# Kernel optimization log

Measured on AMD Instinct MI355X. Metric: run time of the kernel, lower is better.

The kernel has to match this reference:

```python
import jax, jax.numpy as jnp
import numpy as np

D = 512        # latent_dim
DT = 256       # text_latent_dim
H = 8          # num_heads
TE = 2048      # time_embed_dim
NEG = -1000000.0


def _ln(x, g, b, eps=1e-5):
    m = jnp.mean(x, axis=-1, keepdims=True)
    v = jnp.mean(jnp.square(x - m), axis=-1, keepdims=True)
    return (x - m) * jax.lax.rsqrt(v + eps) * g + b


def _linear(x, W, b):
    return x @ W.T + b


def setup_inputs() -> dict:
    key = jax.random.key(0)
    ks = jax.random.split(key, 24)
    B, T, NT, R, LR = 32, 1024, 77, 4, 256
    inp = {
        'x': jax.random.normal(ks[0], (B, T, D), jnp.float32),
        'xf': jax.random.normal(ks[1], (B, NT, DT), jnp.float32),
        'emb': jax.random.normal(ks[2], (B, TE), jnp.float32),
        'src_mask': jax.random.randint(ks[3], (B, T, 1), 0, 2).astype(jnp.float32),
        'cond_type': jax.random.randint(ks[4], (B, 1, 1), 0, 100).astype(jnp.int32),
        're_motion': jax.random.normal(ks[5], (B, R, LR, D), jnp.float32),
        're_text': jax.random.normal(ks[6], (B, R, 1, D), jnp.float32),
        're_mask': jax.random.randint(ks[7], (B, R, LR), 0, 2).astype(jnp.float32),
    }
    s = 0.02
    def W(k, o, i):
        return jax.random.normal(k, (o, i), jnp.float32) * s
    params = {
        'norm_g': jnp.ones((D,), jnp.float32), 'norm_b': jnp.zeros((D,), jnp.float32),
        'tnorm_g': jnp.ones((DT,), jnp.float32), 'tnorm_b': jnp.zeros((DT,), jnp.float32),
        'rn1_g': jnp.ones((2 * D,), jnp.float32), 'rn1_b': jnp.zeros((2 * D,), jnp.float32),
        'rn2_g': jnp.ones((D,), jnp.float32), 'rn2_b': jnp.zeros((D,), jnp.float32),
        'Wq': W(ks[8], D, D), 'bq': jnp.zeros((D,), jnp.float32),
        'Wkt': W(ks[9], D, DT), 'bkt': jnp.zeros((D,), jnp.float32),
        'Wvt': W(ks[10], D, DT), 'bvt': jnp.zeros((D,), jnp.float32),
        'Wkm': W(ks[11], D, D), 'bkm': jnp.zeros((D,), jnp.float32),
        'Wvm': W(ks[12], D, D), 'bvm': jnp.zeros((D,), jnp.float32),
        'Wkr': W(ks[13], D, 2 * D), 'bkr': jnp.zeros((D,), jnp.float32),
        'Wvr': W(ks[14], D, D), 'bvr': jnp.zeros((D,), jnp.float32),
        'emb_W': W(ks[15], 2 * D, TE), 'emb_b': jnp.zeros((2 * D,), jnp.float32),
        'snorm_g': jnp.ones((D,), jnp.float32), 'snorm_b': jnp.zeros((D,), jnp.float32),
        'out_W': W(ks[16], D, D), 'out_b': jnp.zeros((D,), jnp.float32),
    }
    inp.update(params)
    return inp


def _forward(x, xf, emb, src_mask, cond_type, re_motion, re_text, re_mask,
             norm_g, norm_b, tnorm_g, tnorm_b, rn1_g, rn1_b, rn2_g, rn2_b,
             Wq, bq, Wkt, bkt, Wvt, bvt, Wkm, bkm, Wvm, bvm, Wkr, bkr, Wvr, bvr,
             emb_W, emb_b, snorm_g, snorm_b, out_W, out_b):
    B, T, _ = x.shape
    re_mask_r = re_mask.reshape(B, -1, 1)                       # [B, R*LR, 1]
    N = xf.shape[1] + T + re_motion.shape[1] * re_motion.shape[2]

    xn = _ln(x, norm_g, norm_b)                                  # [B,T,D]
    xfn = _ln(xf, tnorm_g, tnorm_b)                              # [B,NT,DT]
    query = _linear(xn, Wq, bq)                                  # [B,T,D]

    text_ct = (cond_type % 10 > 0).astype(x.dtype)               # [B,1,1]
    retr_ct = (cond_type // 10 > 0).astype(x.dtype)              # [B,1,1]

    re_text_rep = jnp.broadcast_to(re_text, re_motion.shape)     # repeat along Lr
    re_feat_key = jnp.concatenate([re_motion, re_text_rep], axis=-1).reshape(B, -1, 2 * D)

    k_text = _linear(xfn, Wkt, bkt) + (1.0 - text_ct) * NEG
    k_retr = (_linear(_ln(re_feat_key, rn1_g, rn1_b), Wkr, bkr)
              + (1.0 - retr_ct) * NEG + (1.0 - re_mask_r) * NEG)
    k_mot = _linear(xn, Wkm, bkm) + (1.0 - src_mask) * NEG
    key_cat = jnp.concatenate([k_text, k_retr, k_mot], axis=1)   # [B,N,D]

    q = jax.nn.softmax(query.reshape(B, T, H, -1), axis=-1)      # softmax over head_dim
    k = jax.nn.softmax(key_cat.reshape(B, N, H, -1), axis=1)     # softmax over tokens

    re_feat_value = re_motion.reshape(B, -1, D)
    v_text = _linear(xfn, Wvt, bvt) * text_ct
    v_retr = _linear(_ln(re_feat_value, rn2_g, rn2_b), Wvr, bvr) * retr_ct * re_mask_r
    v_mot = _linear(xn, Wvm, bvm) * src_mask
    v = jnp.concatenate([v_text, v_retr, v_mot], axis=1).reshape(B, N, H, -1)

    attention = jnp.einsum('bnhd,bnhl->bhdl', k, v)              # [B,H,hd,hd]
    y = jnp.einsum('bthd,bhdl->bthl', q, attention).reshape(B, T, D)

    # StylizationBlock: film-style scale/shift from time embedding, zero-init out proj
    emb_out = _linear(jax.nn.silu(emb), emb_W, emb_b)[:, None, :]  # [B,1,2D]
    scale, shift = emb_out[..., :D], emb_out[..., D:]
    h = _ln(y, snorm_g, snorm_b) * (1.0 + scale) + shift
    h = _linear(jax.nn.silu(h), out_W, out_b)
    return x + h


def reference(x, xf, emb, src_mask, cond_type, re_motion, re_text, re_mask,
              norm_g, norm_b, tnorm_g, tnorm_b, rn1_g, rn1_b, rn2_g, rn2_b,
              Wq, bq, Wkt, bkt, Wvt, bvt, Wkm, bkm, Wvm, bvm, Wkr, bkr, Wvr, bvr,
              emb_W, emb_b, snorm_g, snorm_b, out_W, out_b):
    return _forward(x, xf, emb, src_mask, cond_type, re_motion, re_text, re_mask,
                    norm_g, norm_b, tnorm_g, tnorm_b, rn1_g, rn1_b, rn2_g, rn2_b,
                    Wq, bq, Wkt, bkt, Wvt, bvt, Wkm, bkm, Wvm, bvm, Wkr, bkr, Wvr, bvr,
                    emb_W, emb_b, snorm_g, snorm_b, out_W, out_b)
```

## Files before the change

### kernel.cpp

```cpp
#include <hip/hip_runtime.h>
#include <cstddef>
#include <cstdint>

#define DEV __device__ __forceinline__

namespace {

constexpr int kH = 8;
constexpr int kB = 32, kT = 1024, kNT = 77, kR = 4, kLR = 256;
constexpr int kRL = kR * kLR;
constexpr float kNEG = -1000000.0f;
constexpr int kNtot = 2304;
constexpr int kNS2 = 3;

typedef __bf16 bf16x8 __attribute__((ext_vector_type(8)));
typedef float f32x4 __attribute__((ext_vector_type(4)));

DEV unsigned short f2bf(float f) {
  unsigned int u = __float_as_uint(f);
  u += 0x7fffu + ((u >> 16) & 1u);
  return (unsigned short)(u >> 16);
}
DEV float bf2f(unsigned short h) { return __uint_as_float(((unsigned int)h) << 16); }

DEV float wave_sum(float v) {
  #pragma unroll
  for (int s = 32; s; s >>= 1) v += __shfl_xor(v, s);
  return v;
}

template<int COLS>
__global__ __launch_bounds__(256) void ln_bf16(const float* __restrict__ in,
    const float* __restrict__ g, const float* __restrict__ be,
    unsigned short* __restrict__ out) {
  constexpr int PT = COLS / 256;
  int row = blockIdx.x;
  const float* p = in + (size_t)row * COLS;
  unsigned short* o = out + (size_t)row * COLS;
  float v[PT]; float s = 0.f, s2 = 0.f;
  #pragma unroll
  for (int i = 0; i < PT; i++) {
    v[i] = p[threadIdx.x + i * 256];
    s += v[i]; s2 += v[i] * v[i];
  }
  __shared__ float red[2][4];
  int lane = threadIdx.x & 63, w = threadIdx.x >> 6;
  s = wave_sum(s); s2 = wave_sum(s2);
  if (!lane) { red[0][w] = s; red[1][w] = s2; }
  __syncthreads();
  s = red[0][0] + red[0][1] + red[0][2] + red[0][3];
  s2 = red[1][0] + red[1][1] + red[1][2] + red[1][3];
  float mean = s / COLS;
  float var = s2 / COLS - mean * mean;
  float rstd = rsqrtf(var + 1e-5f);
  #pragma unroll
  for (int i = 0; i < PT; i++) {
    int c = threadIdx.x + i * 256;
    o[c] = f2bf((v[i] - mean) * rstd * g[c] + be[c]);
  }
}

__global__ __launch_bounds__(256) void rfk_stats(const float* __restrict__ mot,
    const float* __restrict__ txt, unsigned short* __restrict__ mot_bf,
    float* __restrict__ s1k, float* __restrict__ s2k,
    float* __restrict__ s1v, float* __restrict__ s2v) {
  int m = blockIdx.x;
  const float* pm = mot + (size_t)m * 512;
  const float* pt = txt + (size_t)(m >> 8) * 512;
  float v[2], t[2];
  float sv = 0.f, sv2 = 0.f, st = 0.f, st2 = 0.f;
  #pragma unroll
  for (int i = 0; i < 2; i++) {
    v[i] = pm[threadIdx.x + i * 256]; sv += v[i]; sv2 += v[i] * v[i];
    t[i] = pt[threadIdx.x + i * 256]; st += t[i]; st2 += t[i] * t[i];
  }
  __shared__ float red[4][4];
  int lane = threadIdx.x & 63, w = threadIdx.x >> 6;
  sv = wave_sum(sv); sv2 = wave_sum(sv2); st = wave_sum(st); st2 = wave_sum(st2);
  if (!lane) { red[0][w] = sv; red[1][w] = sv2; red[2][w] = st; red[3][w] = st2; }
  __syncthreads();
  #pragma unroll
  for (int i = 0; i < 2; i++)
    mot_bf[(size_t)m * 512 + threadIdx.x + i * 256] = f2bf(v[i]);
  if (threadIdx.x == 0) {
    float SV = red[0][0] + red[0][1] + red[0][2] + red[0][3];
    float SV2 = red[1][0] + red[1][1] + red[1][2] + red[1][3];
    float ST = red[2][0] + red[2][1] + red[2][2] + red[2][3];
    float ST2 = red[3][0] + red[3][1] + red[3][2] + red[3][3];
    float SA = SV + ST, SA2 = SV2 + ST2;
    float ma = SA / 1024.f, va = SA2 / 1024.f - ma * ma;
    float ra = rsqrtf(va + 1e-5f);
    float mv = SV / 512.f, vv = SV2 / 512.f - mv * mv;
    float rv = rsqrtf(vv + 1e-5f);
    s1k[m] = ra; s2k[m] = -ra * ma;
    s1v[m] = rv; s2v[m] = -rv * mv;
  }
}

__global__ __launch_bounds__(256) void prep_w(
    const float* __restrict__ Wkr, const float* __restrict__ g1,
    const float* __restrict__ b1, const float* __restrict__ bkr,
    const float* __restrict__ Wvr, const float* __restrict__ g2,
    const float* __restrict__ b2, const float* __restrict__ bvr,
    unsigned short* __restrict__ w1lo, unsigned short* __restrict__ w2,
    float* __restrict__ G1, float* __restrict__ B1,
    float* __restrict__ G2, float* __restrict__ B2) {
  int n = blockIdx.x;
  int tid = threadIdx.x;
  float gs = 0.f, bs = 0.f;
  #pragma unroll
  for (int i = 0; i < 4; i++) {
    int k = tid + i * 256;
    float w = Wkr[(size_t)n * 1024 + k];
    float gv = g1[k];
    gs += gv * w; bs += b1[k] * w;
    if (i < 2) w1lo[(size_t)n * 512 + k] = f2bf(gv * w);
  }
  float g2s = 0.f, b2s = 0.f;
  #pragma unroll
  for (int i = 0; i < 2; i++) {
    int k = tid + i * 256;
    float w = Wvr[(size_t)n * 512 + k];
    g2s += g2[k] * w; b2s += b2[k] * w;
    w2[(size_t)n * 512 + k] = f2bf(g2[k] * w);
  }
  __shared__ float red[4][4];
  int lane = tid & 63, w_ = tid >> 6;
  gs = wave_sum(gs); bs = wave_sum(bs); g2s = wave_sum(g2s); b2s = wave_sum(b2s);
  if (!lane) { red[0][w_] = gs; red[1][w_] = bs; red[2][w_] = g2s; red[3][w_] = b2s; }
  __syncthreads();
  if (tid == 0) {
    G1[n] = red[0][0] + red[0][1] + red[0][2] + red[0][3];
    B1[n] = red[1][0] + red[1][1] + red[1][2] + red[1][3] + bkr[n];
    G2[n] = red[2][0] + red[2][1] + red[2][2] + red[2][3];
    B2[n] = red[3][0] + red[3][1] + red[3][2] + red[3][3] + bvr[n];
  }
}

__global__ __launch_bounds__(256) void text_T(const float* __restrict__ re_text,
    const float* __restrict__ g1, const float* __restrict__ Wkr,
    float* __restrict__ T) {
  int m = blockIdx.x;
  int ns = blockIdx.y;
  __shared__ float tr[512];
  int tid = threadIdx.x;
  #pragma unroll
  for (int i = 0; i < 2; i++) {
    int k = tid + i * 256;
    tr[k] = re_text[(size_t)m * 512 + k] * g1[512 + k];
  }
  __syncthreads();
  int n = ns * 64 + (tid >> 2);
  int k0 = (tid & 3) * 128;
  const float* wp = Wkr + (size_t)n * 1024 + 512 + k0;
  float acc = 0.f;
  #pragma unroll
  for (int k = 0; k < 128; k += 4) {
    float4 w4 = *reinterpret_cast<const float4*>(wp + k);
    float4 t4 = *reinterpret_cast<const float4*>(&tr[k0 + k]);
    acc = fmaf(t4.x, w4.x, fmaf(t4.y, w4.y, fmaf(t4.z, w4.z, fmaf(t4.w, w4.w, acc))));
  }
  acc += __shfl_xor(acc, 1);
  acc += __shfl_xor(acc, 2);
  if ((tid & 3) == 0) T[(size_t)m * 512 + n] = acc;
}

__global__ __launch_bounds__(256) void rowmask_kernel(const int* __restrict__ ct,
    const float* __restrict__ src_mask, const float* __restrict__ re_mask,
    float* __restrict__ kaT, float* __restrict__ kaR, float* __restrict__ kaM,
    float* __restrict__ vmT, float* __restrict__ vmR, float* __restrict__ vmM,
    int nB) {
  int i = blockIdx.x * 256 + threadIdx.x;
  if (i < nB * kRL) {
    int b = i >> 10;
    int c = ct[b];
    float retr = (c / 10 > 0) ? 1.f : 0.f;
    float rm = re_mask[i];
    kaR[i] = (1.f - retr) * kNEG + (1.f - rm) * kNEG;
    vmR[i] = retr * rm;
    float sm = src_mask[i];
    kaM[i] = (1.f - sm) * kNEG;
    vmM[i] = sm;
  }
  if (i < nB * kNT) {
    int b = i / kNT;
    int c = ct[b];
    float text = (c % 10 > 0) ? 1.f : 0.f;
    kaT[i] = (1.f - text) * kNEG;
    vmT[i] = text;
  }
}

__global__ __launch_bounds__(256) void castw(const float* __restrict__ s,
    unsigned short* __restrict__ d, int n) {
  int i = (blockIdx.x * 256 + threadIdx.x) * 4;
  if (i < n) {
    float4 v = *reinterpret_cast<const float4*>(s + i);
    ushort4 o;
    o.x = f2bf(v.x); o.y = f2bf(v.y); o.z = f2bf(v.z); o.w = f2bf(v.w);
    *reinterpret_cast<ushort4*>(d + i) = o;
  }
}

__global__ __launch_bounds__(256) void zpad_kernel(unsigned short* __restrict__ E,
    unsigned short* __restrict__ V, int rows) {
  int i = blockIdx.x * 256 + threadIdx.x;
  if (i >= rows * 24) return;
  int row = i / 24, c = i % 24;
  size_t off = (size_t)row * kNtot + 2112 + c * 8;
  ulonglong2 z; z.x = 0; z.y = 0;
  *reinterpret_cast<ulonglong2*>(E + off) = z;
  *reinterpret_cast<ulonglong2*>(V + off) = z;
}

__global__ __launch_bounds__(256) void silu_emb(const float* __restrict__ emb,
    float* __restrict__ semb) {
  int i = (blockIdx.x * 256 + threadIdx.x) * 4;
  float4 v = *reinterpret_cast<const float4*>(emb + i);
  float4 o;
  o.x = v.x / (1.f + __expf(-v.x));
  o.y = v.y / (1.f + __expf(-v.y));
  o.z = v.z / (1.f + __expf(-v.z));
  o.w = v.w / (1.f + __expf(-v.w));
  *reinterpret_cast<float4*>(semb + i) = o;
}

__global__ __launch_bounds__(256) void emb_gemv2(const float* __restrict__ semb,
    const float* __restrict__ W, float* __restrict__ part) {
  int n = blockIdx.x * 4 + (threadIdx.x >> 6);
  int s = blockIdx.y;
  int lane = threadIdx.x & 63;
  int k = s * 256 + lane * 4;
  float4 wv = *reinterpret_cast<const float4*>(&W[(size_t)n * 2048 + k]);
  float acc[32];
  #pragma unroll
  for (int m = 0; m < 32; m++) {
    float4 sv = *reinterpret_cast<const float4*>(&semb[(size_t)m * 2048 + k]);
    acc[m] = fmaf(sv.x, wv.x, fmaf(sv.y, wv.y, fmaf(sv.z, wv.z, sv.w * wv.w)));
  }
  #pragma unroll
  for (int m = 0; m < 32; m++) {
    float t = wave_sum(acc[m]);
    if (lane == 0) part[((size_t)s * 32 + m) * 1024 + n] = t;
  }
}
__global__ __launch_bounds__(256) void emb_fin(const float* __restrict__ part,
    const float* __restrict__ bias, float* __restrict__ ss) {
  int i = blockIdx.x * 256 + threadIdx.x;
  float s = 0.f;
  #pragma unroll
  for (int c = 0; c < 8; c++) s += part[(size_t)c * 32768 + i];
  ss[i] = s + bias[i & 1023];
}

__global__ __launch_bounds__(256) void res_kernel(const unsigned short* __restrict__ c,
    const float* __restrict__ x, float* __restrict__ out, int n4) {
  for (int i = blockIdx.x * 256 + threadIdx.x; i < n4; i += gridDim.x * 256) {
    int j = i * 4;
    ushort4 cv = *reinterpret_cast<const ushort4*>(c + j);
    float4 xv = *reinterpret_cast<const float4*>(x + j);
    float4 o;
    o.x = xv.x + bf2f(cv.x); o.y = xv.y + bf2f(cv.y);
    o.z = xv.z + bf2f(cv.z); o.w = xv.w + bf2f(cv.w);
    *reinterpret_cast<float4*>(out + j) = o;
  }
}

template<int OUTMODE, int TR, int EPI>
__global__ __launch_bounds__(256) void gemm_mfma(
    const unsigned short* __restrict__ A, const unsigned short* __restrict__ W,
    const float* __restrict__ bias, void* __restrict__ Cout,
    int M, int K, int m_per_b, int n_total, int out_off,
    const float* __restrict__ rowAdd, const float* __restrict__ rowMul,
    const float* __restrict__ s1, const float* __restrict__ s2,
    const float* __restrict__ Gv, const float* __restrict__ Tt) {
  __shared__ __align__(16) char smem[32768];
  unsigned short* lds = (unsigned short*)smem;
  const int tid = threadIdx.x;
  const int lane = tid & 63;
  const int wv = tid >> 6;
  const int wr = (wv >> 1) * 64;
  const int wc = (wv & 1) * 64;
  const int m0 = blockIdx.y * 128;
  const int n0 = blockIdx.x * 128;

  const unsigned short* srcA[2]; const unsigned short* srcB[2];
  int dstOff[2];
  #pragma unroll
  for (int i = 0; i < 2; i++) {
    int lin = i * 256 + tid;
    int r = lin >> 2, cl = lin & 3;
    int cs = cl ^ ((r >> 1) & 3);
    int ra = m0 + r; if (ra > M - 1) ra = M - 1;
    srcA[i] = A + (size_t)ra * K + cs * 8;
    srcB[i] = W + (size_t)(n0 + r) * K + cs * 8;
    dstOff[i] = lin * 8;
  }
  int offA[4], offB[4];
  #pragma unroll
  for (int i = 0; i < 4; i++) {
    int r = wr + i * 16 + (lane & 15);
    int c = (lane >> 4) ^ ((r >> 1) & 3);
    offA[i] = r * 32 + c * 8;
    int rb = wc + i * 16 + (lane & 15);
    int cb = (lane >> 4) ^ ((rb >> 1) & 3);
    offB[i] = rb * 32 + cb * 8;
  }

  f32x4 acc[4][4] = {};

  #pragma unroll
  for (int i = 0; i < 2; i++) {
    __builtin_amdgcn_global_load_lds(
        (const __attribute__((address_space(1))) void*)(srcA[i]),
        (__attribute__((address_space(3))) void*)&lds[dstOff[i]], 16, 0, 0);
    __builtin_amdgcn_global_load_lds(
        (const __attribute__((address_space(1))) void*)(srcB[i]),
        (__attribute__((address_space(3))) void*)&lds[4096 + dstOff[i]], 16, 0, 0);
  }
  __syncthreads();

  int c = 0;
  for (int k0 = 0; k0 < K; k0 += 32) {
    int nc = c ^ 1;
    if (k0 + 32 < K) {
      #pragma unroll
      for (int i = 0; i < 2; i++) {
        __builtin_amdgcn_global_load_lds(
            (const __attribute__((address_space(1))) void*)(srcA[i] + k0 + 32),
            (__attribute__((address_space(3))) void*)&lds[nc * 8192 + dstOff[i]], 16, 0, 0);
        __builtin_amdgcn_global_load_lds(
            (const __attribute__((address_space(1))) void*)(srcB[i] + k0 + 32),
            (__attribute__((address_space(3))) void*)&lds[nc * 8192 + 4096 + dstOff[i]], 16, 0, 0);
      }
    }
    bf16x8 af[4], bf[4];
    #pragma unroll
    for (int i = 0; i < 4; i++) {
      af[i] = *reinterpret_cast<const bf16x8*>(&lds[c * 8192 + offA[i]]);
      bf[i] = *reinterpret_cast<const bf16x8*>(&lds[c * 8192 + 4096 + offB[i]]);
    }
    #pragma unroll
    for (int i = 0; i < 4; i++)
      #pragma unroll
      for (int j = 0; j < 4; j++)
        acc[i][j] = __builtin_amdgcn_mfma_f32_16x16x32_bf16(af[i], bf[j], acc[i][j], 0, 0, 0);
    __syncthreads();
    c = nc;
  }

  const int r4 = (lane >> 4) << 2;
  const int colb = n0 + wc + (lane & 15);
  const int rowb = m0 + wr + r4;

  auto epival = [&](float accv, int rowg, int col) -> float {
    float v;
    if (EPI == 1) {
      v = (accv + Tt[(size_t)(rowg >> 8) * 512 + col]) * s1[rowg]
          + s2[rowg] * Gv[col] + bias[col] + rowAdd[rowg];
    } else if (EPI == 2) {
      v = (accv * s1[rowg] + s2[rowg] * Gv[col] + bias[col]) * rowMul[rowg];
    } else {
      float ra = rowAdd ? rowAdd[rowg] : 0.f;
      float rm = rowMul ? rowMul[rowg] : 1.f;
      v = (accv + bias[col] + ra) * rm;
    }
    if (OUTMODE == 2) v = __expf(v);
    return v;
  };

  if (TR && (m_per_b & 7)) {
    unsigned short* C16 = (unsigned short*)Cout;
    #pragma unroll
    for (int i = 0; i < 4; i++) {
      #pragma unroll
      for (int r = 0; r < 4; r++) {
        int row = rowb + i * 16 + r;
        if (row >= M) continue;
        size_t nn = out_off + (row % m_per_b);
        size_t cb = (size_t)(row / m_per_b) * 512;
        #pragma unroll
        for (int j = 0; j < 4; j++) {
          int col = colb + j * 16;
          C16[(cb + col) * kNtot + nn] = f2bf(epival(acc[i][j][r], row, col));
        }
      }
    }
    return;
  }

  unsigned short* S = (unsigned short*)smem;
  #pragma unroll
  for (int i = 0; i < 4; i++) {
    #pragma unroll
    for (int r = 0; r < 4; r++) {
      int row_t = wr + i * 16 + r4 + r;
      int rowg = m0 + row_t; if (rowg > M - 1) rowg = M - 1;
      int key = ((row_t >> 3) & 7) << 3;
      #pragma unroll
      for (int j = 0; j < 4; j++) {
        int col_t = wc + j * 16 + (lane & 15);
        S[row_t * 128 + (col_t ^ key)] = f2bf(epival(acc[i][j][r], rowg, n0 + col_t));
      }
    }
  }
  __syncthreads();
  if (TR) {
    #pragma unroll
    for (int it = 0; it < 8; it++) {
      int slot = it * 256 + tid;
      int col_t = slot >> 4;
      int mcx = slot & 15;
      int mc = mcx * 8;
      int key = (mcx & 7) << 3;
      union { unsigned short u[8]; ulonglong2 v; } w;
      #pragma unroll
      for (int e = 0; e < 8; e++)
        w.u[e] = S[(mc + e) * 128 + (col_t ^ key)];
      int row = m0 + mc;
      size_t obase = ((size_t)(row / m_per_b) * 512 + n0 + col_t) * (size_t)kNtot
                   + out_off + (row % m_per_b);
      *reinterpret_cast<ulonglong2*>((unsigned short*)Cout + obase) = w.v;
    }
  } else {
    #pragma unroll
    for (int it = 0; it < 8; it++) {
      int slot = it * 256 + tid;
      int row_t = slot >> 4;
      int cs = (slot & 15) * 8;
      int key = ((row_t >> 3) & 7) << 3;
      int row = m0 + row_t;
      if (row < M) {
        size_t orow = (size_t)(row / m_per_b) * n_total + out_off + (row % m_per_b);
        ulonglong2 d = *reinterpret_cast<const ulonglong2*>(&S[row_t * 128 + (cs ^ key)]);
        *reinterpret_cast<ulonglong2*>((unsigned short*)Cout + orow * 512 + n0 + cs) = d;
      }
    }
  }
}

__global__ __launch_bounds__(256) void attp_kernel(const unsigned short* __restrict__ E,
    const unsigned short* __restrict__ V, float* __restrict__ part,
    float* __restrict__ part_cs) {
  int bh = blockIdx.x;
  int s = blockIdx.y;
  const unsigned short* Ep = E + (size_t)bh * 64 * kNtot;
  const unsigned short* Vp = V + (size_t)bh * 64 * kNtot;
  __shared__ __align__(16) char smem[34816];
  unsigned short* Elds = (unsigned short*)smem;
  unsigned short* Vlds = (unsigned short*)(smem + 17408);
  int tid = threadIdx.x, lane = tid & 63, wv = tid >> 6;
  f32x4 acc[4] = {};
  float csum = 0.f;
  int cd = tid & 63, cq = tid >> 6;
  const int arow = (wv * 16 + (lane & 15)) * 136 + ((lane >> 4) << 3);
  const int brow0 = ((lane & 15)) * 136 + ((lane >> 4) << 3);

  for (int it = 0; it < 6; it++) {
    int n0 = s * 768 + it * 128;
    __syncthreads();
    #pragma unroll
    for (int r = 0; r < 4; r++) {
      int ch = r * 256 + tid;
      int d = ch >> 4, off = (ch & 15) * 8;
      *reinterpret_cast<ulonglong2*>(&Elds[d * 136 + off]) =
          *reinterpret_cast<const ulonglong2*>(Ep + (size_t)d * kNtot + n0 + off);
      *reinterpret_cast<ulonglong2*>(&Vlds[d * 136 + off]) =
          *reinterpret_cast<const ulonglong2*>(Vp + (size_t)d * kNtot + n0 + off);
    }
    __syncthreads();
    #pragma unroll
    for (int ks = 0; ks < 4; ks++) {
      bf16x8 af = *reinterpret_cast<const bf16x8*>(&Elds[arow + ks * 32]);
      #pragma unroll
      for (int j = 0; j < 4; j++) {
        bf16x8 bf = *reinterpret_cast<const bf16x8*>(&Vlds[brow0 + j * 16 * 136 + ks * 32]);
        acc[j] = __builtin_amdgcn_mfma_f32_16x16x32_bf16(af, bf, acc[j], 0, 0, 0);
      }
    }
    #pragma unroll
    for (int k8 = 0; k8 < 4; k8++) {
      bf16x8 ev = *reinterpret_cast<const bf16x8*>(&Elds[cd * 136 + cq * 32 + k8 * 8]);
      const unsigned short* pu = reinterpret_cast<const unsigned short*>(&ev);
      #pragma unroll
      for (int e = 0; e < 8; e++) csum += bf2f(pu[e]);
    }
  }
  float* op = part + ((size_t)bh * kNS2 + s) * 4096;
  int dbase = wv * 16 + ((lane >> 4) << 2);
  #pragma unroll
  for (int j = 0; j < 4; j++)
    #pragma unroll
    for (int r = 0; r < 4; r++)
      op[(dbase + r) * 64 + j * 16 + (lane & 15)] = acc[j][r];
  __syncthreads();
  float* csu = (float*)smem;
  csu[cq * 64 + cd] = csum;
  __syncthreads();
  if (tid < 64)
    part_cs[((size_t)bh * kNS2 + s) * 64 + tid] =
        csu[tid] + csu[64 + tid] + csu[128 + tid] + csu[192 + tid];
}

__global__ __launch_bounds__(256) void attc_kernel(const float* __restrict__ part,
    const float* __restrict__ part_cs, unsigned short* __restrict__ attT) {
  int bh = blockIdx.x;
  __shared__ float at[64][65];
  __shared__ float sinv[64];
  int tid = threadIdx.x;
  if (tid < 64) {
    float s = 0.f;
    #pragma unroll
    for (int c = 0; c < kNS2; c++) s += part_cs[((size_t)bh * kNS2 + c) * 64 + tid];
    sinv[tid] = 1.f / s;
  }
  for (int i = tid; i < 4096; i += 256) {
    float s = 0.f;
    #pragma unroll
    for (int c = 0; c < kNS2; c++) s += part[((size_t)bh * kNS2 + c) * 4096 + i];
    at[i >> 6][i & 63] = s;
  }
  __syncthreads();
  for (int j = tid; j < 4096; j += 256) {
    int l = j >> 6, d = j & 63;
    attT[(size_t)bh * 4096 + j] = f2bf(at[d][l] * sinv[d]);
  }
}

__global__ __launch_bounds__(256) void y_mfma(const unsigned short* __restrict__ q,
    const unsigned short* __restrict__ attT, unsigned short* __restrict__ y) {
  int bh = blockIdx.x; int b = bh >> 3, h = bh & 7;
  int t0 = blockIdx.y * 128;
  __shared__ unsigned short bt[64][72];
  __shared__ float rs[128];
  __shared__ unsigned short ob[128][72];
  int tid = threadIdx.x, lane = tid & 63, wv = tid >> 6;
  int wr = wv * 32;
  for (int i = tid; i < 512; i += 256) {
    int row = i >> 3, c8 = (i & 7) * 8;
    *reinterpret_cast<ulonglong2*>(&bt[row][c8]) =
        *reinterpret_cast<const ulonglong2*>(attT + (size_t)bh * 4096 + row * 64 + c8);
  }
  const unsigned short* qp = q + ((size_t)(b * 1024 + t0 + wr)) * 512 + h * 64;
  bf16x8 af[2][2];
  #pragma unroll
  for (int i = 0; i < 2; i++) {
    int row = i * 16 + (lane & 15);
    #pragma unroll
    for (int s = 0; s < 2; s++)
      af[i][s] = *reinterpret_cast<const bf16x8*>(qp + (size_t)row * 512 + s * 32 + (lane >> 4) * 8);
  }
  #pragma unroll
  for (int i = 0; i < 2; i++) {
    float r = 0.f;
    #pragma unroll
    for (int s = 0; s < 2; s++) {
      const unsigned short* pu = reinterpret_cast<const unsigned short*>(&af[i][s]);
      #pragma unroll
      for (int e = 0; e < 8; e++) r += bf2f(pu[e]);
    }
    r += __shfl_xor(r, 16); r += __shfl_xor(r, 32);
    if (lane < 16) rs[wr + i * 16 + lane] = r;
  }
  __syncthreads();
  f32x4 acc[2][4] = {};
  #pragma unroll
  for (int s = 0; s < 2; s++) {
    #pragma unroll
    for (int j = 0; j < 4; j++) {
      bf16x8 bf = *reinterpret_cast<const bf16x8*>(&bt[j * 16 + (lane & 15)][s * 32 + (lane >> 4) * 8]);
      #pragma unroll
      for (int i = 0; i < 2; i++)
        acc[i][j] = __builtin_amdgcn_mfma_f32_16x16x32_bf16(af[i][s], bf, acc[i][j], 0, 0, 0);
    }
  }
  int r4 = (lane >> 4) << 2;
  #pragma unroll
  for (int i = 0; i < 2; i++) {
    #pragma unroll
    for (int r = 0; r < 4; r++) {
      int row = wr + i * 16 + r4 + r;
      float rinv = 1.f / rs[row];
      #pragma unroll
      for (int j = 0; j < 4; j++)
        ob[row][j * 16 + (lane & 15)] = f2bf(acc[i][j][r] * rinv);
    }
  }
  __syncthreads();
  for (int i = tid; i < 1024; i += 256) {
    int row = i >> 3, c8 = (i & 7) * 8;
    *reinterpret_cast<ulonglong2*>(y + ((size_t)(b * 1024 + t0 + row)) * 512 + h * 64 + c8) =
        *reinterpret_cast<const ulonglong2*>(&ob[row][c8]);
  }
}

__global__ __launch_bounds__(256) void mod_kernel(const unsigned short* __restrict__ y,
    const float* __restrict__ ss, const float* __restrict__ g, const float* __restrict__ be,
    unsigned short* __restrict__ h) {
  int row = blockIdx.x; int b = row >> 10;
  const unsigned short* p = y + (size_t)row * 512;
  unsigned short* o = h + (size_t)row * 512;
  float v[2]; float s = 0.f, s2 = 0.f;
  #pragma unroll
  for (int i = 0; i < 2; i++) {
    v[i] = bf2f(p[threadIdx.x + i * 256]);
    s += v[i]; s2 += v[i] * v[i];
  }
  __shared__ float red[2][4];
  int lane = threadIdx.x & 63, w = threadIdx.x >> 6;
  s = wave_sum(s); s2 = wave_sum(s2);
  if (!lane) { red[0][w] = s; red[1][w] = s2; }
  __syncthreads();
  s = red[0][0] + red[0][1] + red[0][2] + red[0][3];
  s2 = red[1][0] + red[1][1] + red[1][2] + red[1][3];
  float mean = s / 512.f, var = s2 / 512.f - mean * mean;
  float rstd = rsqrtf(var + 1e-5f);
  #pragma unroll
  for (int i = 0; i < 2; i++) {
    int c = threadIdx.x + i * 256;
    float val = (v[i] - mean) * rstd * g[c] + be[c];
    val = val * (1.f + ss[b * 1024 + c]) + ss[b * 1024 + 512 + c];
    o[c] = f2bf(val / (1.f + __expf(-val)));
  }
}

}

extern "C" void kernel_launch(void* const* d_in, const int* in_sizes, int n_in,
                              void* d_out, int out_size, void* d_ws, size_t ws_size,
                              hipStream_t stream) {
  const float* x        = (const float*)d_in[0];
  const float* xf       = (const float*)d_in[1];
  const float* emb      = (const float*)d_in[2];
  const float* src_mask = (const float*)d_in[3];
  const int*   cond     = (const int*)d_in[4];
  const float* re_motion= (const float*)d_in[5];
  const float* re_text  = (const float*)d_in[6];
  const float* re_mask  = (const float*)d_in[7];
  const float* norm_g = (const float*)d_in[8],  * norm_b = (const float*)d_in[9];
  const float* tnorm_g= (const float*)d_in[10], * tnorm_b= (const float*)d_in[11];
  const float* rn1_g  = (const float*)d_in[12], * rn1_b  = (const float*)d_in[13];
  const float* rn2_g  = (const float*)d_in[14], * rn2_b  = (const float*)d_in[15];
  const float* Wq  = (const float*)d_in[16], * bq  = (const float*)d_in[17];
  const float* Wkt = (const float*)d_in[18], * bkt = (const float*)d_in[19];
  const float* Wvt = (const float*)d_in[20], * bvt = (const float*)d_in[21];
  const float* Wkm = (const float*)d_in[22], * bkm = (const float*)d_in[23];
  const float* Wvm = (const float*)d_in[24], * bvm = (const float*)d_in[25];
  const float* Wkr = (const float*)d_in[26], * bkr = (const float*)d_in[27];
  const float* Wvr = (const float*)d_in[28], * bvr = (const float*)d_in[29];
  const float* emb_W = (const float*)d_in[30], * emb_b = (const float*)d_in[31];
  const float* snorm_g = (const float*)d_in[32], * snorm_b = (const float*)d_in[33];
  const float* out_W = (const float*)d_in[34], * out_b = (const float*)d_in[35];
  float* out = (float*)d_out;

  char* base = (char*)d_ws;
  size_t off = 0;
  auto ab = [&](size_t nb) { char* p = base + off; off = (off + nb + 255) & ~(size_t)255; return p; };

  unsigned short* wq_bf  = (unsigned short*)ab(512 * 512 * 2);
  unsigned short* wkt_bf = (unsigned short*)ab(512 * 256 * 2);
  unsigned short* wvt_bf = (unsigned short*)ab(512 * 256 * 2);
  unsigned short* wkm_bf = (unsigned short*)ab(512 * 512 * 2);
  unsigned short* wvm_bf = (unsigned short*)ab(512 * 512 * 2);
  unsigned short* wout_bf= (unsigned short*)ab(512 * 512 * 2);
  unsigned short* w1lo_bf= (unsigned short*)ab(512 * 512 * 2);
  unsigned short* w2_bf  = (unsigned short*)ab(512 * 512 * 2);
  float* G1 = (float*)ab(512 * 4); float* B1 = (float*)ab(512 * 4);
  float* G2 = (float*)ab(512 * 4); float* B2 = (float*)ab(512 * 4);
  float* Tbuf = (float*)ab((size_t)kB * kR * 512 * 4);
  float* semb_f   = (float*)ab((size_t)kB * 2048 * 4);
  float* part_emb = (float*)ab((size_t)8 * kB * 1024 * 4);
  float* ssb_full = (float*)ab((size_t)kB * 1024 * 4);
  float* kaT_full = (float*)ab((size_t)kB * kNT * 4);
  float* vmT_full = (float*)ab((size_t)kB * kNT * 4);
  float* kaR_full = (float*)ab((size_t)kB * kRL * 4);
  float* kaM_full = (float*)ab((size_t)kB * kT * 4);
  float* vmR_full = (float*)ab((size_t)kB * kRL * 4);
  float* vmM_full = (float*)ab((size_t)kB * kT * 4);
  const size_t fixed_off = off;

  auto pad = [](size_t n) { return (n + 255) & ~(size_t)255; };
  auto att_bytes = [&](size_t CH) -> size_t {
    return pad(CH * 8 * 4096 * 2)
         + pad(CH * 8 * (size_t)kNS2 * 4096 * 4)
         + pad(CH * 8 * (size_t)kNS2 * 64 * 4);
  };
  auto chunk_bytes = [&](size_t CH) -> size_t {
    size_t xnr = pad(CH * 1024 * 512 * 2);
    if (att_bytes(CH) > xnr) xnr = att_bytes(CH);
    size_t s = 0;
    s += xnr;
    s += pad(CH * kNT * 256 * 2);
    s += pad(CH * 1024 * 512 * 2);
    s += 4 * pad(CH * 1024 * 4);
    s += pad(CH * 1024 * 512 * 2);
    s += pad((size_t)CH * 512 * kNtot * 2);
    s += pad((size_t)CH * 512 * kNtot * 2);
    return s;
  };
  int CH = 32;
  while (CH > 1 && fixed_off + chunk_bytes(CH) > ws_size) CH >>= 1;

  auto cl = [&](const float* s, unsigned short* d, int n) {
    castw<<<dim3((n / 4 + 255) / 256), 256, 0, stream>>>(s, d, n);
  };
  cl(Wq,  wq_bf,  512 * 512);
  cl(Wkt, wkt_bf, 512 * 256);
  cl(Wvt, wvt_bf, 512 * 256);
  cl(Wkm, wkm_bf, 512 * 512);
  cl(Wvm, wvm_bf, 512 * 512);
  cl(out_W, wout_bf, 512 * 512);
  prep_w<<<dim3(512), 256, 0, stream>>>(Wkr, rn1_g, rn1_b, bkr, Wvr, rn2_g, rn2_b, bvr,
                                        w1lo_bf, w2_bf, G1, B1, G2, B2);
  text_T<<<dim3(kB * kR, 8), 256, 0, stream>>>(re_text, rn1_g, Wkr, Tbuf);

  rowmask_kernel<<<dim3(kB * 4), 256, 0, stream>>>(cond, src_mask, re_mask,
      kaT_full, kaR_full, kaM_full, vmT_full, vmR_full, vmM_full, kB);
  silu_emb<<<dim3(kB * 2048 / 1024), 256, 0, stream>>>(emb, semb_f);
  emb_gemv2<<<dim3(256, 8), 256, 0, stream>>>(semb_f, emb_W, part_emb);
  emb_fin<<<dim3(128), 256, 0, stream>>>(part_emb, emb_b, ssb_full);

  for (int b0 = 0; b0 < kB; b0 += CH) {
    off = fixed_off;
    const int MRc = CH * 1024;
    const int MTc = CH * kNT;

    size_t xnr = pad((size_t)MRc * 512 * 2);
    if (att_bytes(CH) > xnr) xnr = att_bytes(CH);
    char* xnR = ab(xnr);
    unsigned short* xn_bf  = (unsigned short*)xnR;
    unsigned short* attT = (unsigned short*)xnR;
    float* attp = (float*)(xnR + pad((size_t)CH * 8 * 4096 * 2));
    float* part_cs = (float*)(xnR + pad((size_t)CH * 8 * 4096 * 2)
                                  + pad((size_t)CH * 8 * (size_t)kNS2 * 4096 * 4));
    unsigned short* h_bf = xn_bf;

    unsigned short* xfn_bf = (unsigned short*)ab((size_t)MTc * 256 * 2);
    unsigned short* mot_bf = (unsigned short*)ab((size_t)MRc * 512 * 2);
    float* s1k = (float*)ab((size_t)CH * 1024 * 4);
    float* s2k = (float*)ab((size_t)CH * 1024 * 4);
    float* s1v = (float*)ab((size_t)CH * 1024 * 4);
    float* s2v = (float*)ab((size_t)CH * 1024 * 4);
    unsigned short* qb_bf  = (unsigned short*)ab((size_t)MRc * 512 * 2);
    unsigned short* kc_bf  = (unsigned short*)ab((size_t)CH * 512 * kNtot * 2);
    unsigned short* vb_bf  = (unsigned short*)ab((size_t)CH * 512 * kNtot * 2);
    unsigned short* yb16 = mot_bf;
    unsigned short* cfin = qb_bf;

    const float* x_c   = x + (size_t)b0 * kT * 512;
    const float* xf_c  = xf + (size_t)b0 * kNT * 256;
    const float* rm_c  = re_motion + (size_t)b0 * kRL * 512;
    const float* rt_c  = re_text + (size_t)b0 * kR * 512;
    float* out_c = out + (size_t)b0 * kT * 512;

    ln_bf16<512><<<dim3(MRc), 256, 0, stream>>>(x_c, norm_g, norm_b, xn_bf);
    ln_bf16<256><<<dim3(MTc), 256, 0, stream>>>(xf_c, tnorm_g, tnorm_b, xfn_bf);
    rfk_stats<<<dim3(MRc), 256, 0, stream>>>(rm_c, rt_c, mot_bf, s1k, s2k, s1v, s2v);
    zpad_kernel<<<dim3(CH * 48), 256, 0, stream>>>(kc_bf, vb_bf, CH * 512);

    gemm_mfma<2, 0, 0><<<dim3(4, CH * 8), 256, 0, stream>>>(xn_bf, wq_bf, bq, qb_bf,
        MRc, 512, MRc, 0, 0, nullptr, nullptr, nullptr, nullptr, nullptr, nullptr);
    gemm_mfma<2, 1, 0><<<dim3(4, (MTc + 127) / 128), 256, 0, stream>>>(xfn_bf, wkt_bf, bkt, kc_bf,
        MTc, 256, kNT, 0, 0, kaT_full + (size_t)b0 * kNT, nullptr,
        nullptr, nullptr, nullptr, nullptr);
    gemm_mfma<2, 1, 1><<<dim3(4, CH * 8), 256, 0, stream>>>(mot_bf, w1lo_bf, B1, kc_bf,
        MRc, 512, kRL, 0, kNT, kaR_full + (size_t)b0 * kRL, nullptr,
        s1k, s2k, G1, Tbuf + (size_t)b0 * kR * 512);
    gemm_mfma<2, 1, 0><<<dim3(4, CH * 8), 256, 0, stream>>>(xn_bf, wkm_bf, bkm, kc_bf,
        MRc, 512, kT, 0, kNT + kRL, kaM_full + (size_t)b0 * kT, nullptr,
        nullptr, nullptr, nullptr, nullptr);
    gemm_mfma<1, 1, 0><<<dim3(4, (MTc + 127) / 128), 256, 0, stream>>>(xfn_bf, wvt_bf, bvt, vb_bf,
        MTc, 256, kNT, 0, 0, nullptr, vmT_full + (size_t)b0 * kNT,
        nullptr, nullptr, nullptr, nullptr);
    gemm_mfma<1, 1, 2><<<dim3(4, CH * 8), 256, 0, stream>>>(mot_bf, w2_bf, B2, vb_bf,
        MRc, 512, kRL, 0, kNT, nullptr, vmR_full + (size_t)b0 * kRL,
        s1v, s2v, G2, nullptr);
    gemm_mfma<1, 1, 0><<<dim3(4, CH * 8), 256, 0, stream>>>(xn_bf, wvm_bf, bvm, vb_bf,
        MRc, 512, kT, 0, kNT + kRL, nullptr, vmM_full + (size_t)b0 * kT,
        nullptr, nullptr, nullptr, nullptr);

    attp_kernel<<<dim3(CH * 8, kNS2), 256, 0, stream>>>(kc_bf, vb_bf, attp, part_cs);
    attc_kernel<<<dim3(CH * 8), 256, 0, stream>>>(attp, part_cs, attT);
    y_mfma<<<dim3(CH * 8, 8), 256, 0, stream>>>(qb_bf, attT, yb16);

    mod_kernel<<<dim3(MRc), 256, 0, stream>>>(yb16, ssb_full + (size_t)b0 * 1024,
                                              snorm_g, snorm_b, h_bf);
    gemm_mfma<1, 0, 0><<<dim3(4, CH * 8), 256, 0, stream>>>(h_bf, wout_bf, out_b, cfin,
        MRc, 512, MRc, 0, 0, nullptr, nullptr, nullptr, nullptr, nullptr, nullptr);
    res_kernel<<<dim3(2048), 256, 0, stream>>>(cfin, x_c, out_c, MRc * 128);
  }
}
```

Baseline: 563.8 us.

## Fuse projection GEMMs sharing an input into concatenated-weight launches

Concatenates the weights of projections that share the same activation input (Q/Km/Vm on the normalized motion, K/V retrieval on the motion features, K/V text on the text features). Each group becomes one wider GEMM whose column section picks the per-section epilogue and output buffer. This cuts seven GEMM launches to three and gives each launch a larger grid, in exchange for a templated kernel with section-dependent branching. The output GEMM gets a separate, simplified kernel. The A tile is still reloaded for each N tile, so the reuse gain is mostly from fewer launches and fuller grids.

```diff
diff --git a/kernel.cpp b/kernel.cpp
--- a/kernel.cpp
+++ b/kernel.cpp
@@ -266,14 +266,19 @@
   }
 }
 
-template<int OUTMODE, int TR, int EPI>
-__global__ __launch_bounds__(256) void gemm_mfma(
+template<int COMBO>
+__global__ __launch_bounds__(256) void gemm_fused(
     const unsigned short* __restrict__ A, const unsigned short* __restrict__ W,
-    const float* __restrict__ bias, void* __restrict__ Cout,
-    int M, int K, int m_per_b, int n_total, int out_off,
-    const float* __restrict__ rowAdd, const float* __restrict__ rowMul,
-    const float* __restrict__ s1, const float* __restrict__ s2,
-    const float* __restrict__ Gv, const float* __restrict__ Tt) {
+    int M, int K, int m_per_b, int out_off,
+    unsigned short* __restrict__ qout,
+    unsigned short* __restrict__ E, unsigned short* __restrict__ V,
+    const float* __restrict__ biasA, const float* __restrict__ biasB,
+    const float* __restrict__ biasC,
+    const float* __restrict__ rowAddK, const float* __restrict__ rowMulV,
+    const float* __restrict__ s1k, const float* __restrict__ s2k,
+    const float* __restrict__ s1v, const float* __restrict__ s2v,
+    const float* __restrict__ G1v, const float* __restrict__ G2v,
+    const float* __restrict__ Tt) {
   __shared__ __align__(16) char smem[32768];
   unsigned short* lds = (unsigned short*)smem;
   const int tid = threadIdx.x;
@@ -283,6 +288,8 @@
   const int wc = (wv & 1) * 64;
   const int m0 = blockIdx.y * 128;
   const int n0 = blockIdx.x * 128;
+  const int sec = n0 >> 9;
+  const int nlo = n0 & 511;
 
   const unsigned short* srcA[2]; const unsigned short* srcB[2];
   int dstOff[2];
@@ -350,27 +357,27 @@
   }
 
   const int r4 = (lane >> 4) << 2;
-  const int colb = n0 + wc + (lane & 15);
   const int rowb = m0 + wr + r4;
 
-  auto epival = [&](float accv, int rowg, int col) -> float {
-    float v;
-    if (EPI == 1) {
-      v = (accv + Tt[(size_t)(rowg >> 8) * 512 + col]) * s1[rowg]
-          + s2[rowg] * Gv[col] + bias[col] + rowAdd[rowg];
-    } else if (EPI == 2) {
-      v = (accv * s1[rowg] + s2[rowg] * Gv[col] + bias[col]) * rowMul[rowg];
+  auto epival = [&](float accv, int rowg, int cl) -> float {
+    if (COMBO == 0) {
+      if (sec == 0) return __expf(accv + biasA[cl]);
+      if (sec == 1) return __expf(accv + biasB[cl] + rowAddK[rowg]);
+      return (accv + biasC[cl]) * rowMulV[rowg];
+    } else if (COMBO == 1) {
+      if (sec == 0)
+        return __expf((accv + Tt[(size_t)(rowg >> 8) * 512 + cl]) * s1k[rowg]
+                      + s2k[rowg] * G1v[cl] + biasA[cl] + rowAddK[rowg]);
+      return (accv * s1v[rowg] + s2v[rowg] * G2v[cl] + biasB[cl]) * rowMulV[rowg];
     } else {
-      float ra = rowAdd ? rowAdd[rowg] : 0.f;
-      float rm = rowMul ? rowMul[rowg] : 1.f;
-      v = (accv + bias[col] + ra) * rm;
-    }
-    if (OUTMODE == 2) v = __expf(v);
-    return v;
+      if (sec == 0) return __expf(accv + biasA[cl] + rowAddK[rowg]);
+      return (accv + biasB[cl]) * rowMulV[rowg];
+    }
   };
 
-  if (TR && (m_per_b & 7)) {
-    unsigned short* C16 = (unsigned short*)Cout;
+  unsigned short* dstEV = (COMBO == 0) ? (sec == 1 ? E : V) : (sec == 0 ? E : V);
+
+  if (COMBO == 2) {
     #pragma unroll
     for (int i = 0; i < 4; i++) {
       #pragma unroll
@@ -381,8 +388,8 @@
         size_t cb = (size_t)(row / m_per_b) * 512;
         #pragma unroll
         for (int j = 0; j < 4; j++) {
-          int col = colb + j * 16;
-          C16[(cb + col) * kNtot + nn] = f2bf(epival(acc[i][j][r], row, col));
+          int cl = nlo + wc + j * 16 + (lane & 15);
+          dstEV[(cb + cl) * kNtot + nn] = f2bf(epival(acc[i][j][r], row, cl));
         }
       }
     }
@@ -400,12 +407,26 @@
       #pragma unroll
       for (int j = 0; j < 4; j++) {
         int col_t = wc + j * 16 + (lane & 15);
-        S[row_t * 128 + (col_t ^ key)] = f2bf(epival(acc[i][j][r], rowg, n0 + col_t));
+        S[row_t * 128 + (col_t ^ key)] = f2bf(epival(acc[i][j][r], rowg, nlo + col_t));
       }
     }
   }
   __syncthreads();
-  if (TR) {
+  bool linear = (COMBO == 0 && sec == 0);
+  if (linear) {
+    #pragma unroll
+    for (int it = 0; it < 8; it++) {
+      int slot = it * 256 + tid;
+      int row_t = slot >> 4;
+      int cs = (slot & 15) * 8;
+      int key = ((row_t >> 3) & 7) << 3;
+      int row = m0 + row_t;
+      if (row < M) {
+        ulonglong2 d = *reinterpret_cast<const ulonglong2*>(&S[row_t * 128 + (cs ^ key)]);
+        *reinterpret_cast<ulonglong2*>(qout + (size_t)row * 512 + nlo + cs) = d;
+      }
+    }
+  } else {
     #pragma unroll
     for (int it = 0; it < 8; it++) {
       int slot = it * 256 + tid;
@@ -418,23 +439,118 @@
       for (int e = 0; e < 8; e++)
         w.u[e] = S[(mc + e) * 128 + (col_t ^ key)];
       int row = m0 + mc;
-      size_t obase = ((size_t)(row / m_per_b) * 512 + n0 + col_t) * (size_t)kNtot
+      size_t obase = ((size_t)(row / m_per_b) * 512 + nlo + col_t) * (size_t)kNtot
                    + out_off + (row % m_per_b);
-      *reinterpret_cast<ulonglong2*>((unsigned short*)Cout + obase) = w.v;
-    }
-  } else {
-    #pragma unroll
-    for (int it = 0; it < 8; it++) {
-      int slot = it * 256 + tid;
-      int row_t = slot >> 4;
-      int cs = (slot & 15) * 8;
+      *reinterpret_cast<ulonglong2*>(dstEV + obase) = w.v;
+    }
+  }
+}
+
+__global__ __launch_bounds__(256) void gemm_mfma(
+    const unsigned short* __restrict__ A, const unsigned short* __restrict__ W,
+    const float* __restrict__ bias, unsigned short* __restrict__ Cout,
+    int M, int K) {
+  __shared__ __align__(16) char smem[32768];
+  unsigned short* lds = (unsigned short*)smem;
+  const int tid = threadIdx.x;
+  const int lane = tid & 63;
+  const int wv = tid >> 6;
+  const int wr = (wv >> 1) * 64;
+  const int wc = (wv & 1) * 64;
+  const int m0 = blockIdx.y * 128;
+  const int n0 = blockIdx.x * 128;
+
+  const unsigned short* srcA[2]; const unsigned short* srcB[2];
+  int dstOff[2];
+  #pragma unroll
+  for (int i = 0; i < 2; i++) {
+    int lin = i * 256 + tid;
+    int r = lin >> 2, cl = lin & 3;
+    int cs = cl ^ ((r >> 1) & 3);
+    int ra = m0 + r; if (ra > M - 1) ra = M - 1;
+    srcA[i] = A + (size_t)ra * K + cs * 8;
+    srcB[i] = W + (size_t)(n0 + r) * K + cs * 8;
+    dstOff[i] = lin * 8;
+  }
+  int offA[4], offB[4];
+  #pragma unroll
+  for (int i = 0; i < 4; i++) {
+    int r = wr + i * 16 + (lane & 15);
+    int c = (lane >> 4) ^ ((r >> 1) & 3);
+    offA[i] = r * 32 + c * 8;
+    int rb = wc + i * 16 + (lane & 15);
+    int cb = (lane >> 4) ^ ((rb >> 1) & 3);
+    offB[i] = rb * 32 + cb * 8;
+  }
+
+  f32x4 acc[4][4] = {};
+
+  #pragma unroll
+  for (int i = 0; i < 2; i++) {
+    __builtin_amdgcn_global_load_lds(
+        (const __attribute__((address_space(1))) void*)(srcA[i]),
+        (__attribute__((address_space(3))) void*)&lds[dstOff[i]], 16, 0, 0);
+    __builtin_amdgcn_global_load_lds(
+        (const __attribute__((address_space(1))) void*)(srcB[i]),
+        (__attribute__((address_space(3))) void*)&lds[4096 + dstOff[i]], 16, 0, 0);
+  }
+  __syncthreads();
+
+  int c = 0;
+  for (int k0 = 0; k0 < K; k0 += 32) {
+    int nc = c ^ 1;
+    if (k0 + 32 < K) {
+      #pragma unroll
+      for (int i = 0; i < 2; i++) {
+        __builtin_amdgcn_global_load_lds(
+            (const __attribute__((address_space(1))) void*)(srcA[i] + k0 + 32),
+            (__attribute__((address_space(3))) void*)&lds[nc * 8192 + dstOff[i]], 16, 0, 0);
+        __builtin_amdgcn_global_load_lds(
+            (const __attribute__((address_space(1))) void*)(srcB[i] + k0 + 32),
+            (__attribute__((address_space(3))) void*)&lds[nc * 8192 + 4096 + dstOff[i]], 16, 0, 0);
+      }
+    }
+    bf16x8 af[4], bf[4];
+    #pragma unroll
+    for (int i = 0; i < 4; i++) {
+      af[i] = *reinterpret_cast<const bf16x8*>(&lds[c * 8192 + offA[i]]);
+      bf[i] = *reinterpret_cast<const bf16x8*>(&lds[c * 8192 + 4096 + offB[i]]);
+    }
+    #pragma unroll
+    for (int i = 0; i < 4; i++)
+      #pragma unroll
+      for (int j = 0; j < 4; j++)
+        acc[i][j] = __builtin_amdgcn_mfma_f32_16x16x32_bf16(af[i], bf[j], acc[i][j], 0, 0, 0);
+    __syncthreads();
+    c = nc;
+  }
+
+  const int r4 = (lane >> 4) << 2;
+  unsigned short* S = (unsigned short*)smem;
+  #pragma unroll
+  for (int i = 0; i < 4; i++) {
+    #pragma unroll
+    for (int r = 0; r < 4; r++) {
+      int row_t = wr + i * 16 + r4 + r;
       int key = ((row_t >> 3) & 7) << 3;
-      int row = m0 + row_t;
-      if (row < M) {
-        size_t orow = (size_t)(row / m_per_b) * n_total + out_off + (row % m_per_b);
-        ulonglong2 d = *reinterpret_cast<const ulonglong2*>(&S[row_t * 128 + (cs ^ key)]);
-        *reinterpret_cast<ulonglong2*>((unsigned short*)Cout + orow * 512 + n0 + cs) = d;
+      #pragma unroll
+      for (int j = 0; j < 4; j++) {
+        int col_t = wc + j * 16 + (lane & 15);
+        S[row_t * 128 + (col_t ^ key)] = f2bf(acc[i][j][r] + bias[n0 + col_t]);
       }
+    }
+  }
+  __syncthreads();
+  #pragma unroll
+  for (int it = 0; it < 8; it++) {
+    int slot = it * 256 + tid;
+    int row_t = slot >> 4;
+    int cs = (slot & 15) * 8;
+    int key = ((row_t >> 3) & 7) << 3;
+    int row = m0 + row_t;
+    if (row < M) {
+      ulonglong2 d = *reinterpret_cast<const ulonglong2*>(&S[row_t * 128 + (cs ^ key)]);
+      *reinterpret_cast<ulonglong2*>(Cout + (size_t)row * 512 + n0 + cs) = d;
     }
   }
 }
@@ -657,14 +773,10 @@
   size_t off = 0;
   auto ab = [&](size_t nb) { char* p = base + off; off = (off + nb + 255) & ~(size_t)255; return p; };
 
-  unsigned short* wq_bf  = (unsigned short*)ab(512 * 512 * 2);
-  unsigned short* wkt_bf = (unsigned short*)ab(512 * 256 * 2);
-  unsigned short* wvt_bf = (unsigned short*)ab(512 * 256 * 2);
-  unsigned short* wkm_bf = (unsigned short*)ab(512 * 512 * 2);
-  unsigned short* wvm_bf = (unsigned short*)ab(512 * 512 * 2);
+  unsigned short* wcat0 = (unsigned short*)ab((size_t)1536 * 512 * 2);
+  unsigned short* wcat1 = (unsigned short*)ab((size_t)1024 * 512 * 2);
+  unsigned short* wcat2 = (unsigned short*)ab((size_t)1024 * 256 * 2);
   unsigned short* wout_bf= (unsigned short*)ab(512 * 512 * 2);
-  unsigned short* w1lo_bf= (unsigned short*)ab(512 * 512 * 2);
-  unsigned short* w2_bf  = (unsigned short*)ab(512 * 512 * 2);
   float* G1 = (float*)ab(512 * 4); float* B1 = (float*)ab(512 * 4);
   float* G2 = (float*)ab(512 * 4); float* B2 = (float*)ab(512 * 4);
   float* Tbuf = (float*)ab((size_t)kB * kR * 512 * 4);
@@ -704,14 +816,14 @@
   auto cl = [&](const float* s, unsigned short* d, int n) {
     castw<<<dim3((n / 4 + 255) / 256), 256, 0, stream>>>(s, d, n);
   };
-  cl(Wq,  wq_bf,  512 * 512);
-  cl(Wkt, wkt_bf, 512 * 256);
-  cl(Wvt, wvt_bf, 512 * 256);
-  cl(Wkm, wkm_bf, 512 * 512);
-  cl(Wvm, wvm_bf, 512 * 512);
+  cl(Wq,  wcat0,              512 * 512);
+  cl(Wkm, wcat0 + 512 * 512,  512 * 512);
+  cl(Wvm, wcat0 + 1024 * 512, 512 * 512);
+  cl(Wkt, wcat2,              512 * 256);
+  cl(Wvt, wcat2 + 512 * 256,  512 * 256);
   cl(out_W, wout_bf, 512 * 512);
   prep_w<<<dim3(512), 256, 0, stream>>>(Wkr, rn1_g, rn1_b, bkr, Wvr, rn2_g, rn2_b, bvr,
-                                        w1lo_bf, w2_bf, G1, B1, G2, B2);
+                                        wcat1, wcat1 + 512 * 512, G1, B1, G2, B2);
   text_T<<<dim3(kB * kR, 8), 256, 0, stream>>>(re_text, rn1_g, Wkr, Tbuf);
 
   rowmask_kernel<<<dim3(kB * 4), 256, 0, stream>>>(cond, src_mask, re_mask,
@@ -758,26 +870,21 @@
     rfk_stats<<<dim3(MRc), 256, 0, stream>>>(rm_c, rt_c, mot_bf, s1k, s2k, s1v, s2v);
     zpad_kernel<<<dim3(CH * 48), 256, 0, stream>>>(kc_bf, vb_bf, CH * 512);
 
-    gemm_mfma<2, 0, 0><<<dim3(4, CH * 8), 256, 0, stream>>>(xn_bf, wq_bf, bq, qb_bf,
-        MRc, 512, MRc, 0, 0, nullptr, nullptr, nullptr, nullptr, nullptr, nullptr);
-    gemm_mfma<2, 1, 0><<<dim3(4, (MTc + 127) / 128), 256, 0, stream>>>(xfn_bf, wkt_bf, bkt, kc_bf,
-        MTc, 256, kNT, 0, 0, kaT_full + (size_t)b0 * kNT, nullptr,
-        nullptr, nullptr, nullptr, nullptr);
-    gemm_mfma<2, 1, 1><<<dim3(4, CH * 8), 256, 0, stream>>>(mot_bf, w1lo_bf, B1, kc_bf,
-        MRc, 512, kRL, 0, kNT, kaR_full + (size_t)b0 * kRL, nullptr,
-        s1k, s2k, G1, Tbuf + (size_t)b0 * kR * 512);
-    gemm_mfma<2, 1, 0><<<dim3(4, CH * 8), 256, 0, stream>>>(xn_bf, wkm_bf, bkm, kc_bf,
-        MRc, 512, kT, 0, kNT + kRL, kaM_full + (size_t)b0 * kT, nullptr,
-        nullptr, nullptr, nullptr, nullptr);
-    gemm_mfma<1, 1, 0><<<dim3(4, (MTc + 127) / 128), 256, 0, stream>>>(xfn_bf, wvt_bf, bvt, vb_bf,
-        MTc, 256, kNT, 0, 0, nullptr, vmT_full + (size_t)b0 * kNT,
-        nullptr, nullptr, nullptr, nullptr);
-    gemm_mfma<1, 1, 2><<<dim3(4, CH * 8), 256, 0, stream>>>(mot_bf, w2_bf, B2, vb_bf,
-        MRc, 512, kRL, 0, kNT, nullptr, vmR_full + (size_t)b0 * kRL,
-        s1v, s2v, G2, nullptr);
-    gemm_mfma<1, 1, 0><<<dim3(4, CH * 8), 256, 0, stream>>>(xn_bf, wvm_bf, bvm, vb_bf,
-        MRc, 512, kT, 0, kNT + kRL, nullptr, vmM_full + (size_t)b0 * kT,
-        nullptr, nullptr, nullptr, nullptr);
+    gemm_fused<0><<<dim3(12, CH * 8), 256, 0, stream>>>(
+        xn_bf, wcat0, MRc, 512, kT, kNT + kRL,
+        qb_bf, kc_bf, vb_bf, bq, bkm, bvm,
+        kaM_full + (size_t)b0 * kT, vmM_full + (size_t)b0 * kT,
+        nullptr, nullptr, nullptr, nullptr, nullptr, nullptr, nullptr);
+    gemm_fused<1><<<dim3(8, CH * 8), 256, 0, stream>>>(
+        mot_bf, wcat1, MRc, 512, kRL, kNT,
+        nullptr, kc_bf, vb_bf, B1, B2, nullptr,
+        kaR_full + (size_t)b0 * kRL, vmR_full + (size_t)b0 * kRL,
+        s1k, s2k, s1v, s2v, G1, G2, Tbuf + (size_t)b0 * kR * 512);
+    gemm_fused<2><<<dim3(8, (MTc + 127) / 128), 256, 0, stream>>>(
+        xfn_bf, wcat2, MTc, 256, kNT, 0,
+        nullptr, kc_bf, vb_bf, bkt, bvt, nullptr,
+        kaT_full + (size_t)b0 * kNT, vmT_full + (size_t)b0 * kNT,
+        nullptr, nullptr, nullptr, nullptr, nullptr, nullptr, nullptr);
 
     attp_kernel<<<dim3(CH * 8, kNS2), 256, 0, stream>>>(kc_bf, vb_bf, attp, part_cs);
     attc_kernel<<<dim3(CH * 8), 256, 0, stream>>>(attp, part_cs, attT);
@@ -785,8 +892,7 @@
 
     mod_kernel<<<dim3(MRc), 256, 0, stream>>>(yb16, ssb_full + (size_t)b0 * 1024,
                                               snorm_g, snorm_b, h_bf);
-    gemm_mfma<1, 0, 0><<<dim3(4, CH * 8), 256, 0, stream>>>(h_bf, wout_bf, out_b, cfin,
-        MRc, 512, MRc, 0, 0, nullptr, nullptr, nullptr, nullptr, nullptr, nullptr);
+    gemm_mfma<<<dim3(4, CH * 8), 256, 0, stream>>>(h_bf, wout_bf, out_b, cfin, MRc, 512);
     res_kernel<<<dim3(2048), 256, 0, stream>>>(cfin, x_c, out_c, MRc * 128);
   }
 }
```

Measured after the change: 526.3 us. 1.07x faster.
